# Performance work log

Measured on AMD Instinct MI355X. Metric: run time of the kernel, lower is better.

Reference implementation:

```python
import jax, jax.numpy as jnp
import numpy as np

N = 4096          # total ensemble boxes per frame
M = 20            # MAX_MERGE_NUMS
H = 16            # MergeNet hidden_c
COND_THRES = 0.2
IOU_THRES = 0.3


def setup_inputs() -> dict:
    key = jax.random.key(0)
    ks = jax.random.split(key, 6)
    u = jax.random.uniform(ks[0], (N, 9), dtype=jnp.float32)
    # realistic lidar boxes: centers in a ~140x80x8m range, dims in [0.5, 4.5), heading in [-pi, pi)
    centers = (u[:, 0:3] - 0.5) * jnp.array([140.0, 80.0, 8.0], jnp.float32)
    dims = u[:, 3:6] * 4.0 + 0.5
    heading = (u[:, 6:7] - 0.5) * (2.0 * np.pi)
    extra = u[:, 7:9]  # extra box attrs (cols 7:9), untouched by merge
    pred_boxes = jnp.concatenate([centers, dims, heading, extra], axis=-1)
    pred_scores = jax.random.uniform(ks[1], (N,), dtype=jnp.float32)
    pred_labels = jax.random.randint(ks[2], (N,), 0, 3)
    w1 = (jax.random.normal(ks[3], (M, H), jnp.float32) / np.sqrt(M)).astype(jnp.float32)
    b1 = jnp.zeros((H,), jnp.float32)
    w2 = (jax.random.normal(ks[4], (H, H), jnp.float32) / np.sqrt(H)).astype(jnp.float32)
    b2 = jnp.zeros((H,), jnp.float32)
    w3 = (jax.random.normal(ks[5], (H, 1), jnp.float32) / np.sqrt(H)).astype(jnp.float32)
    b3 = jnp.zeros((1,), jnp.float32)
    return dict(pred_boxes=pred_boxes, pred_scores=pred_scores, pred_labels=pred_labels,
                w1=w1, b1=b1, w2=w2, b2=b2, w3=w3, b3=b3)


def _bev_aligned(b):
    # boxes3d_lidar_to_aligned_bev_boxes: swap dx/dy when |limit_period(heading)| >= pi/4
    ang = b[..., 6] - jnp.floor(b[..., 6] / np.pi + 0.5) * np.pi
    swap = jnp.abs(ang) >= (np.pi / 4)
    dx = jnp.where(swap, b[..., 4], b[..., 3])
    dy = jnp.where(swap, b[..., 3], b[..., 4])
    return jnp.stack([b[..., 0] - dx / 2, b[..., 1] - dy / 2,
                      b[..., 0] + dx / 2, b[..., 1] + dy / 2], axis=-1)


def _iou_one_many(a, b):
    # axis-aligned BEV IoU of one box a[4] vs many b[N,4]
    xmin = jnp.maximum(a[0], b[:, 0]); ymin = jnp.maximum(a[1], b[:, 1])
    xmax = jnp.minimum(a[2], b[:, 2]); ymax = jnp.minimum(a[3], b[:, 3])
    inter = jnp.maximum(xmax - xmin, 0.0) * jnp.maximum(ymax - ymin, 0.0)
    area_a = (a[2] - a[0]) * (a[3] - a[1])
    area_b = (b[:, 2] - b[:, 0]) * (b[:, 3] - b[:, 1])
    return inter / jnp.maximum(area_a + area_b - inter, 1e-6)


def _nms_merge(pred_boxes, pred_scores, pred_labels, w1, b1, w2, b2, w3, b3):
    valid = pred_scores > COND_THRES
    sort_key = jnp.where(valid, pred_scores, -jnp.inf)
    order = jnp.argsort(-sort_key)                 # descending by score; invalid sink
    boxes9 = pred_boxes[order]
    labels = pred_labels[order]
    scores = pred_scores[order]
    suppressed0 = ~valid[order]
    boxes7 = boxes9[:, :7]
    bev0 = _bev_aligned(boxes7)                    # merged boxes get suppressed, so bev is static

    def mergenet(ob):                              # ob: [M, 7] -> merged box [7]
        x = ob.T                                   # [7, M] (k is the feature axis)
        h = jax.nn.relu(x @ w1 + b1)
        h = jax.nn.relu(h @ w2 + b2)
        return (h @ w3 + b3)[:, 0]

    def step(suppressed, i):
        active = ~suppressed[i]
        same = (labels == labels[i]) & (~suppressed)
        iou = _iou_one_many(bev0[i], bev0)         # [N]
        over = (iou > IOU_THRES) & same            # includes self (iou=1)
        count = jnp.sum(over)
        rank = jnp.cumsum(over) - 1                # slot of each overlap, in score order
        tgt = jnp.where(over & (rank < M), rank, M)
        ob = jnp.zeros((M, 7), boxes7.dtype).at[tgt].set(boxes7, mode='drop')
        bi = boxes7[i]
        new_box = jnp.where(count > 1, mergenet(ob), bi)
        new_box = new_box.at[3:6].set(jnp.maximum(new_box[3:6], 1e-5))
        out_box = jnp.where(active, new_box, bi)
        return suppressed | (over & active), (out_box, active)

    _, (merged7, keep) = jax.lax.scan(step, suppressed0, jnp.arange(N))
    out_boxes = jnp.concatenate([merged7, boxes9[:, 7:9]], axis=-1)   # [N, 9]
    return out_boxes, scores, labels, keep


def reference(pred_boxes, pred_scores, pred_labels, w1, b1, w2, b2, w3, b3):
    # Returns fixed-shape (boxes9, scores, labels, keep_mask); rows with keep=False
    # correspond to boxes that torch's dynamic version would have removed.
    return _nms_merge(pred_boxes, pred_scores, pred_labels, w1, b1, w2, b2, w3, b3)
```

## Files before the change

kernel.cpp:

```cpp
#include <hip/hip_runtime.h>
#include <cstdint>

typedef unsigned long long u64;
typedef unsigned int u32;

#define NB 4096
#define NW 64
#define MM 20
#define HH 16
#define COND_THRES 0.2f
#define IOU_THRES 0.3f
#define PI_F  3.14159265358979323846f
#define PI4_F 0.78539816339744830962f

#define WS_KEPT    0
#define WS_MASK    32768
#define WS_BOX9S   (WS_MASK + NB*NW*8)
#define WS_BEVS    (WS_BOX9S + NB*9*4)
#define WS_SCORES  (WS_BEVS + NB*16)
#define WS_LABELS  (WS_SCORES + NB*4)
#define WS_SUPSTEP (WS_LABELS + NB*4)
#define WS_NBRW    (WS_SUPSTEP + NB*4)
#define WS_PART    (WS_NBRW + NB*8)

__device__ __forceinline__ u64 sort_key(float s, int i) {
  u32 sb = (s > COND_THRES) ? __float_as_uint(s) : 0u;
  return ((u64)(sb ^ 0xFFFFFFFFu) << 12) | (u64)i;
}

__global__ void __launch_bounds__(256) k_rank(const float* __restrict__ scores,
                                              u32* __restrict__ partial,
                                              u64* __restrict__ nbrw) {
  __shared__ u64 kj[256];
  int tid = threadIdx.x;
  int j = blockIdx.y * 256 + tid;
  kj[tid] = sort_key(scores[j], j);
  __syncthreads();
  int i = blockIdx.x * 256 + tid;
  if (blockIdx.y == 0) nbrw[i] = 0;
  u64 ki = sort_key(scores[i], i);
  int cnt = 0;
  #pragma unroll 16
  for (int t = 0; t < 256; ++t) cnt += (kj[t] < ki) ? 1 : 0;
  partial[i * 16 + blockIdx.y] = (u32)cnt;
}

__global__ void __launch_bounds__(256) k_scatter(const u32* __restrict__ partial,
                                                 const float* __restrict__ scores,
                                                 const float* __restrict__ boxes9,
                                                 const int* __restrict__ labels,
                                                 float* __restrict__ box9s, float4* __restrict__ bevs,
                                                 float* __restrict__ scoress, int* __restrict__ labelss) {
  #pragma clang fp contract(off)
  int i = blockIdx.x * 256 + threadIdx.x;
  const uint4* p4 = (const uint4*)(partial + i * 16);
  uint4 a0 = p4[0], a1 = p4[1], a2 = p4[2], a3 = p4[3];
  int r = (int)(a0.x + a0.y + a0.z + a0.w + a1.x + a1.y + a1.z + a1.w +
                a2.x + a2.y + a2.z + a2.w + a3.x + a3.y + a3.z + a3.w);
  float b[9];
  #pragma unroll
  for (int f = 0; f < 9; ++f) b[f] = boxes9[i * 9 + f];
  #pragma unroll
  for (int f = 0; f < 9; ++f) box9s[r * 9 + f] = b[f];
  float ang = b[6] - floorf(b[6] / PI_F + 0.5f) * PI_F;
  bool sw = fabsf(ang) >= PI4_F;
  float dx = sw ? b[4] : b[3];
  float dy = sw ? b[3] : b[4];
  bevs[r] = make_float4(b[0] - dx * 0.5f, b[1] - dy * 0.5f,
                        b[0] + dx * 0.5f, b[1] + dy * 0.5f);
  scoress[r] = scores[i];
  labelss[r] = labels[i];
}

__global__ void __launch_bounds__(64) k_mask(const float4* __restrict__ bevs,
                                             const int* __restrict__ labelss,
                                             const float* __restrict__ scoress,
                                             u64* __restrict__ mask,
                                             u64* __restrict__ nbrw) {
  #pragma clang fp contract(off)
  __shared__ float4 bj[64];
  __shared__ int lj[64];
  int t = threadIdx.x;
  int jt = blockIdx.x;
  int it = blockIdx.y;
  int j = jt * 64 + t;
  bj[t] = bevs[j];
  lj[t] = labelss[j];
  u64 vj = __ballot(scoress[j] > COND_THRES);
  int i = it * 64 + t;
  float4 a = bevs[i];
  int la = labelss[i];
  float area_a = (a.z - a.x) * (a.w - a.y);
  __syncthreads();
  u64 w = 0;
  #pragma unroll 8
  for (int kk = 0; kk < 64; ++kk) {
    float4 bb = bj[kk];
    float xmin = fmaxf(a.x, bb.x), ymin = fmaxf(a.y, bb.y);
    float xmax = fminf(a.z, bb.z), ymax = fminf(a.w, bb.w);
    float inter = fmaxf(xmax - xmin, 0.0f) * fmaxf(ymax - ymin, 0.0f);
    float area_b = (bb.z - bb.x) * (bb.w - bb.y);
    float iou = inter / fmaxf(area_a + area_b - inter, 1e-6f);
    if ((iou > IOU_THRES) && (la == lj[kk])) w |= (1ull << kk);
  }
  mask[(u64)i * NW + jt] = w;
  if (jt <= it) {
    u64 below = (jt < it) ? ~0ull : ((1ull << t) - 1ull);
    if (w & vj & below) atomicOr(&nbrw[i], 1ull << jt);
  }
}

__global__ void __launch_bounds__(1024) k_nms(const u64* __restrict__ mask,
                                              const u64* __restrict__ nbrw,
                                              const float* __restrict__ scoress,
                                              u64* __restrict__ keptOut) {
  __shared__ u64 decided[64], kept[64];
  __shared__ int remaining;
  int tid = threadIdx.x;
  if (tid < 64) {
    u64 v = 0;
    #pragma unroll 8
    for (int b = 0; b < 64; ++b)
      if (scoress[(tid << 6) | b] > COND_THRES) v |= (1ull << b);
    decided[tid] = ~v;
    kept[tid] = 0;
  }
  if (tid == 0) remaining = 0;
  __syncthreads();
  if (tid < 64) atomicAdd(&remaining, __popcll(~decided[tid]));
  u64 cw0[4], cw1[4];
  u32 meta[4];
  #pragma unroll
  for (int s = 0; s < 4; ++s) {
    int i = tid + (s << 10);
    int wi = i >> 6;
    u64 bit = 1ull << (i & 63);
    u64 t = nbrw[i];
    int n = 0; u32 ovf = 0;
    u64 c0 = 0, c1 = 0; u32 i0 = 0, i1 = 0;
    while (t) {
      int w = __builtin_ctzll(t);
      t &= t - 1;
      u64 below = (w < wi) ? ~0ull : (bit - 1ull);
      u64 m = mask[(u64)i * NW + w] & below;
      if (n == 0)      { c0 = m; i0 = (u32)w; }
      else if (n == 1) { c1 = m; i1 = (u32)w; }
      else ovf = 1;
      ++n;
    }
    cw0[s] = c0; cw1[s] = c1;
    meta[s] = i0 | (i1 << 6) | ((u32)(n > 2 ? 2 : n) << 12) | (ovf << 14);
  }
  __syncthreads();
  while (remaining > 0) {
    int decIdx[4]; bool decKept[4]; int nDec = 0;
    #pragma unroll
    for (int s = 0; s < 4; ++s) {
      int i = tid + (s << 10);
      int wi = i >> 6;
      u64 bit = 1ull << (i & 63);
      if (decided[wi] & bit) continue;
      bool hasU = false, hasK = false;
      u32 mt = meta[s];
      if (!(mt & (1u << 14))) {
        int n = (mt >> 12) & 3;
        if (n >= 1) {
          int w = mt & 63;
          hasU = hasU || ((cw0[s] & ~decided[w]) != 0ull);
          hasK = hasK || ((cw0[s] & kept[w]) != 0ull);
        }
        if (n >= 2) {
          int w = (mt >> 6) & 63;
          hasU = hasU || ((cw1[s] & ~decided[w]) != 0ull);
          hasK = hasK || ((cw1[s] & kept[w]) != 0ull);
        }
      } else {
        u64 t = nbrw[i];
        while (t) {
          int w = __builtin_ctzll(t);
          t &= t - 1;
          u64 below = (w < wi) ? ~0ull : (bit - 1ull);
          u64 m = mask[(u64)i * NW + w] & below;
          hasU = hasU || ((m & ~decided[w]) != 0ull);
          hasK = hasK || ((m & kept[w]) != 0ull);
        }
      }
      if (!hasU) { decIdx[nDec] = i; decKept[nDec] = !hasK; ++nDec; }
    }
    __syncthreads();
    for (int d = 0; d < nDec; ++d) {
      int i = decIdx[d];
      u64 bit = 1ull << (i & 63);
      atomicOr(&decided[i >> 6], bit);
      if (decKept[d]) atomicOr(&kept[i >> 6], bit);
      atomicSub(&remaining, 1);
    }
    __syncthreads();
  }
  if (tid < 64) keptOut[tid] = kept[tid];
}

__global__ void __launch_bounds__(256) k_supstep(const u64* __restrict__ mask,
                                                 const u64* __restrict__ kept,
                                                 const float* __restrict__ scoress,
                                                 int* __restrict__ supstep) {
  __shared__ u64 K[64];
  if (threadIdx.x < 64) K[threadIdx.x] = kept[threadIdx.x];
  __syncthreads();
  int j = blockIdx.x * 256 + threadIdx.x;
  if (!(scoress[j] > COND_THRES)) { supstep[j] = -1; return; }
  int res = 0x7FFFFFFF;
  #pragma unroll 4
  for (int w = 0; w < 64; ++w) {
    u64 m = mask[(u64)j * NW + w] & K[w];
    if (m) { res = (w << 6) + __builtin_ctzll(m); break; }
  }
  supstep[j] = res;
}

__global__ void __launch_bounds__(64) k_merge(
    const u64* __restrict__ mask, const int* __restrict__ supstep,
    const float* __restrict__ box9s, const float* __restrict__ scoress,
    const int* __restrict__ labelss,
    const float* __restrict__ w1, const float* __restrict__ b1,
    const float* __restrict__ w2, const float* __restrict__ b2,
    const float* __restrict__ w3, const float* __restrict__ b3,
    float* __restrict__ out) {
  #pragma clang fp contract(off)
  __shared__ int candList[MM];
  __shared__ float ob[MM][7];
  __shared__ float h1[7][HH];
  __shared__ float h2[7][HH];
  __shared__ float res[7];
  int i = blockIdx.x;
  int t = threadIdx.x;
  bool active = (supstep[i] == i);
  u64 wq = 0;
  int cnt = 0;
  if (active) {
    u64 w = mask[(u64)i * NW + t];
    while (w) {
      int b = __builtin_ctzll(w);
      w &= w - 1;
      int j = (t << 6) | b;
      if (supstep[j] >= i) { wq |= (1ull << b); cnt++; }
    }
  }
  int incl = cnt;
  #pragma unroll
  for (int off = 1; off < 64; off <<= 1) {
    int v = __shfl_up(incl, off);
    if (t >= off) incl += v;
  }
  int excl = incl - cnt;
  int count = __shfl(incl, 63);
  bool merged = active && (count > 1);
  if (merged && wq) {
    int pos = excl;
    u64 ww = wq;
    while (ww && pos < MM) {
      int b = __builtin_ctzll(ww);
      ww &= ww - 1;
      candList[pos++] = (t << 6) | b;
    }
  }
  __syncthreads();
  if (merged) {
    int nc = count < MM ? count : MM;
    if (t < MM) {
      if (t < nc) {
        int j = candList[t];
        #pragma unroll
        for (int f = 0; f < 7; ++f) ob[t][f] = box9s[j * 9 + f];
      } else {
        #pragma unroll
        for (int f = 0; f < 7; ++f) ob[t][f] = 0.0f;
      }
    }
    __syncthreads();
    for (int o = t; o < 7 * HH; o += 64) {
      int f = o >> 4, hh = o & 15;
      float acc = b1[hh];
      #pragma unroll
      for (int m = 0; m < MM; ++m) acc += ob[m][f] * w1[m * HH + hh];
      h1[f][hh] = fmaxf(acc, 0.0f);
    }
    __syncthreads();
    for (int o = t; o < 7 * HH; o += 64) {
      int f = o >> 4, oo = o & 15;
      float acc = b2[oo];
      #pragma unroll
      for (int k = 0; k < HH; ++k) acc += h1[f][k] * w2[k * HH + oo];
      h2[f][oo] = fmaxf(acc, 0.0f);
    }
    __syncthreads();
    if (t < 7) {
      float acc = b3[0];
      #pragma unroll
      for (int k = 0; k < HH; ++k) acc += h2[t][k] * w3[k];
      if (t >= 3 && t < 6) acc = fmaxf(acc, 1e-5f);
      res[t] = acc;
    }
    __syncthreads();
  }
  if (t < 9) {
    float v = box9s[i * 9 + t];
    if (merged && t < 7) v = res[t];
    out[i * 9 + t] = v;
  }
  if (t == 0) {
    out[NB * 9 + i]          = scoress[i];
    out[NB * 9 + NB + i]     = (float)labelss[i];
    out[NB * 9 + 2 * NB + i] = active ? 1.0f : 0.0f;
  }
}

extern "C" void kernel_launch(void* const* d_in, const int* in_sizes, int n_in,
                              void* d_out, int out_size, void* d_ws, size_t ws_size,
                              hipStream_t stream) {
  const float* boxes9 = (const float*)d_in[0];
  const float* scores = (const float*)d_in[1];
  const int*   labels = (const int*)d_in[2];
  const float* w1 = (const float*)d_in[3];
  const float* b1 = (const float*)d_in[4];
  const float* w2 = (const float*)d_in[5];
  const float* b2 = (const float*)d_in[6];
  const float* w3 = (const float*)d_in[7];
  const float* b3 = (const float*)d_in[8];
  char* ws = (char*)d_ws;
  u64*    kept    = (u64*)(ws + WS_KEPT);
  u64*    mask    = (u64*)(ws + WS_MASK);
  float*  box9s   = (float*)(ws + WS_BOX9S);
  float4* bevs    = (float4*)(ws + WS_BEVS);
  float*  scoress = (float*)(ws + WS_SCORES);
  int*    labelss = (int*)(ws + WS_LABELS);
  int*    supstep = (int*)(ws + WS_SUPSTEP);
  u64*    nbrw    = (u64*)(ws + WS_NBRW);
  u32*    part    = (u32*)(ws + WS_PART);
  float*  out     = (float*)d_out;

  hipLaunchKernelGGL(k_rank,    dim3(16, 16),   dim3(256),  0, stream, scores, part, nbrw);
  hipLaunchKernelGGL(k_scatter, dim3(NB / 256), dim3(256),  0, stream, part, scores, boxes9, labels,
                     box9s, bevs, scoress, labelss);
  hipLaunchKernelGGL(k_mask,    dim3(64, 64),   dim3(64),   0, stream, bevs, labelss, scoress,
                     mask, nbrw);
  hipLaunchKernelGGL(k_nms,     dim3(1),        dim3(1024), 0, stream, mask, nbrw, scoress, kept);
  hipLaunchKernelGGL(k_supstep, dim3(NB / 256), dim3(256),  0, stream, mask, kept, scoress, supstep);
  hipLaunchKernelGGL(k_merge,   dim3(NB),       dim3(64),   0, stream, mask, supstep,
                     box9s, scoress, labelss, w1, b1, w2, b2, w3, b3, out);
}
```

Measured before the change: 132.4 us.

## Replace atomic NMS iteration with wave ballots and drop supstep kernel

The single-block NMS loop now computes decisions per wave with __ballot and keeps its own decided/kept words in registers. Lane 0 of each wave publishes them once per round, and a per-wave pending flag ends the loop, replacing per-element shared atomics and a shared remaining counter. The separate supstep kernel is removed: k_merge reads the kept bitmask and, for each overlapping candidate, checks in place whether a kept box of higher rank suppresses it. This saves one launch and the atomic traffic in the serial NMS loop, at the cost of extra mask row reads inside k_merge for each neighbour.

Result: faster. 117.6 us (-11.1%).

```diff
diff --git a/kernel.cpp b/kernel.cpp
--- a/kernel.cpp
+++ b/kernel.cpp
@@ -19,8 +19,7 @@
 #define WS_BEVS    (WS_BOX9S + NB*9*4)
 #define WS_SCORES  (WS_BEVS + NB*16)
 #define WS_LABELS  (WS_SCORES + NB*4)
-#define WS_SUPSTEP (WS_LABELS + NB*4)
-#define WS_NBRW    (WS_SUPSTEP + NB*4)
+#define WS_NBRW    (WS_LABELS + NB*4)
 #define WS_PART    (WS_NBRW + NB*8)
 
 __device__ __forceinline__ u64 sort_key(float s, int i) {
@@ -115,19 +114,25 @@
                                               const float* __restrict__ scoress,
                                               u64* __restrict__ keptOut) {
   __shared__ u64 decided[64], kept[64];
-  __shared__ int remaining;
+  __shared__ int wavePending[16];
+  __shared__ int anyPending;
   int tid = threadIdx.x;
-  if (tid < 64) {
-    u64 v = 0;
-    #pragma unroll 8
-    for (int b = 0; b < 64; ++b)
-      if (scoress[(tid << 6) | b] > COND_THRES) v |= (1ull << b);
-    decided[tid] = ~v;
-    kept[tid] = 0;
-  }
-  if (tid == 0) remaining = 0;
-  __syncthreads();
-  if (tid < 64) atomicAdd(&remaining, __popcll(~decided[tid]));
+  int lane = tid & 63;
+  int waveId = tid >> 6;
+  u64 dcache[4], kcache[4];
+  #pragma unroll
+  for (int s = 0; s < 4; ++s) {
+    int i = tid + (s << 10);
+    bool v = scoress[i] > COND_THRES;
+    u64 vw = __ballot(v);
+    dcache[s] = ~vw;
+    kcache[s] = 0;
+    if (lane == 0) {
+      int wi = waveId + (s << 4);
+      decided[wi] = ~vw;
+      kept[wi] = 0;
+    }
+  }
   u64 cw0[4], cw1[4];
   u32 meta[4];
   #pragma unroll
@@ -152,74 +157,77 @@
     meta[s] = i0 | (i1 << 6) | ((u32)(n > 2 ? 2 : n) << 12) | (ovf << 14);
   }
   __syncthreads();
-  while (remaining > 0) {
-    int decIdx[4]; bool decKept[4]; int nDec = 0;
+  while (true) {
+    bool pend = false;
     #pragma unroll
     for (int s = 0; s < 4; ++s) {
-      int i = tid + (s << 10);
-      int wi = i >> 6;
-      u64 bit = 1ull << (i & 63);
-      if (decided[wi] & bit) continue;
-      bool hasU = false, hasK = false;
-      u32 mt = meta[s];
-      if (!(mt & (1u << 14))) {
-        int n = (mt >> 12) & 3;
-        if (n >= 1) {
-          int w = mt & 63;
-          hasU = hasU || ((cw0[s] & ~decided[w]) != 0ull);
-          hasK = hasK || ((cw0[s] & kept[w]) != 0ull);
+      bool mine_und = !((dcache[s] >> lane) & 1ull);
+      bool dec = false, keepme = false;
+      if (mine_und) {
+        bool hasU = false, hasK = false;
+        u32 mt = meta[s];
+        if (!(mt & (1u << 14))) {
+          int n = (mt >> 12) & 3;
+          if (n >= 1) {
+            int w = mt & 63;
+            u64 dw = decided[w], kw = kept[w];
+            hasU = (cw0[s] & ~dw) != 0ull;
+            hasK = (cw0[s] & kw) != 0ull;
+          }
+          if (n >= 2) {
+            int w = (mt >> 6) & 63;
+            u64 dw = decided[w], kw = kept[w];
+            hasU = hasU || ((cw1[s] & ~dw) != 0ull);
+            hasK = hasK || ((cw1[s] & kw) != 0ull);
+          }
+        } else {
+          int i = tid + (s << 10);
+          int wi = i >> 6;
+          u64 bit = 1ull << (i & 63);
+          u64 t = nbrw[i];
+          while (t) {
+            int w = __builtin_ctzll(t);
+            t &= t - 1;
+            u64 below = (w < wi) ? ~0ull : (bit - 1ull);
+            u64 m = mask[(u64)i * NW + w] & below;
+            hasU = hasU || ((m & ~decided[w]) != 0ull);
+            hasK = hasK || ((m & kept[w]) != 0ull);
+          }
         }
-        if (n >= 2) {
-          int w = (mt >> 6) & 63;
-          hasU = hasU || ((cw1[s] & ~decided[w]) != 0ull);
-          hasK = hasK || ((cw1[s] & kept[w]) != 0ull);
-        }
-      } else {
-        u64 t = nbrw[i];
-        while (t) {
-          int w = __builtin_ctzll(t);
-          t &= t - 1;
-          u64 below = (w < wi) ? ~0ull : (bit - 1ull);
-          u64 m = mask[(u64)i * NW + w] & below;
-          hasU = hasU || ((m & ~decided[w]) != 0ull);
-          hasK = hasK || ((m & kept[w]) != 0ull);
-        }
+        dec = !hasU;
+        keepme = !hasK;
       }
-      if (!hasU) { decIdx[nDec] = i; decKept[nDec] = !hasK; ++nDec; }
-    }
-    __syncthreads();
-    for (int d = 0; d < nDec; ++d) {
-      int i = decIdx[d];
-      u64 bit = 1ull << (i & 63);
-      atomicOr(&decided[i >> 6], bit);
-      if (decKept[d]) atomicOr(&kept[i >> 6], bit);
-      atomicSub(&remaining, 1);
-    }
-    __syncthreads();
+      u64 b_nd = __ballot(dec);
+      u64 b_nk = __ballot(dec && keepme);
+      dcache[s] |= b_nd;
+      kcache[s] |= b_nk;
+      pend |= (mine_und && !dec);
+    }
+    u64 pw = __ballot(pend);
+    if (lane == 0) wavePending[waveId] = (pw != 0ull) ? 1 : 0;
+    __syncthreads();
+    if (lane == 0) {
+      #pragma unroll
+      for (int s = 0; s < 4; ++s) {
+        int wi = waveId + (s << 4);
+        decided[wi] = dcache[s];
+        kept[wi] = kcache[s];
+      }
+    }
+    if (tid == 0) {
+      int any = 0;
+      #pragma unroll
+      for (int w = 0; w < 16; ++w) any |= wavePending[w];
+      anyPending = any;
+    }
+    __syncthreads();
+    if (!anyPending) break;
   }
   if (tid < 64) keptOut[tid] = kept[tid];
 }
 
-__global__ void __launch_bounds__(256) k_supstep(const u64* __restrict__ mask,
-                                                 const u64* __restrict__ kept,
-                                                 const float* __restrict__ scoress,
-                                                 int* __restrict__ supstep) {
-  __shared__ u64 K[64];
-  if (threadIdx.x < 64) K[threadIdx.x] = kept[threadIdx.x];
-  __syncthreads();
-  int j = blockIdx.x * 256 + threadIdx.x;
-  if (!(scoress[j] > COND_THRES)) { supstep[j] = -1; return; }
-  int res = 0x7FFFFFFF;
-  #pragma unroll 4
-  for (int w = 0; w < 64; ++w) {
-    u64 m = mask[(u64)j * NW + w] & K[w];
-    if (m) { res = (w << 6) + __builtin_ctzll(m); break; }
-  }
-  supstep[j] = res;
-}
-
 __global__ void __launch_bounds__(64) k_merge(
-    const u64* __restrict__ mask, const int* __restrict__ supstep,
+    const u64* __restrict__ mask, const u64* __restrict__ keptG,
     const float* __restrict__ box9s, const float* __restrict__ scoress,
     const int* __restrict__ labelss,
     const float* __restrict__ w1, const float* __restrict__ b1,
@@ -232,18 +240,28 @@
   __shared__ float h1[7][HH];
   __shared__ float h2[7][HH];
   __shared__ float res[7];
+  __shared__ u64 K[64];
   int i = blockIdx.x;
   int t = threadIdx.x;
-  bool active = (supstep[i] == i);
+  K[t] = keptG[t];
+  __syncthreads();
+  bool active = (K[i >> 6] >> (i & 63)) & 1ull;
   u64 wq = 0;
   int cnt = 0;
   if (active) {
     u64 w = mask[(u64)i * NW + t];
+    int hiw = i >> 6;
+    u64 below = (1ull << (i & 63)) - 1ull;
     while (w) {
       int b = __builtin_ctzll(w);
       w &= w - 1;
       int j = (t << 6) | b;
-      if (supstep[j] >= i) { wq |= (1ull << b); cnt++; }
+      if (scoress[j] > COND_THRES) {
+        const u64* rowj = mask + (u64)j * NW;
+        u64 found = rowj[hiw] & K[hiw] & below;
+        for (int ww = 0; ww < hiw; ++ww) found |= rowj[ww] & K[ww];
+        if (!found) { wq |= (1ull << b); cnt++; }
+      }
     }
   }
   int incl = cnt;
@@ -334,7 +352,6 @@
   float4* bevs    = (float4*)(ws + WS_BEVS);
   float*  scoress = (float*)(ws + WS_SCORES);
   int*    labelss = (int*)(ws + WS_LABELS);
-  int*    supstep = (int*)(ws + WS_SUPSTEP);
   u64*    nbrw    = (u64*)(ws + WS_NBRW);
   u32*    part    = (u32*)(ws + WS_PART);
   float*  out     = (float*)d_out;
@@ -345,7 +362,6 @@
   hipLaunchKernelGGL(k_mask,    dim3(64, 64),   dim3(64),   0, stream, bevs, labelss, scoress,
                      mask, nbrw);
   hipLaunchKernelGGL(k_nms,     dim3(1),        dim3(1024), 0, stream, mask, nbrw, scoress, kept);
-  hipLaunchKernelGGL(k_supstep, dim3(NB / 256), dim3(256),  0, stream, mask, kept, scoress, supstep);
-  hipLaunchKernelGGL(k_merge,   dim3(NB),       dim3(64),   0, stream, mask, supstep,
+  hipLaunchKernelGGL(k_merge,   dim3(NB),       dim3(64),   0, stream, mask, kept,
                      box9s, scoress, labelss, w1, b1, w2, b2, w3, b3, out);
 }
```
